# Kernel tuning notes

Hardware: AMD Instinct MI355X
Metric: run time of the kernel (lower is better)

## Reference

```python
import jax, jax.numpy as jnp
import numpy as np

N = 50000        # nodes
E = 400000       # edges
SC = 64          # scalar (l=0) channels
VC = 32          # vector (l=1) channels
DIM = SC + 3 * VC  # 160
NB = 64          # radial basis functions
CUTOFF = 5.0
EPS = 1e-5


def _edge_rot_mat(edge_vec, edge_rand):
    # init_edge_rot_mat: build per-edge frame aligning edge dir with canonical axis
    dist = jnp.sqrt(jnp.sum(edge_vec ** 2, axis=1, keepdims=True))
    nx = edge_vec / dist
    ev2 = edge_rand - 0.5
    ev2 = ev2 / jnp.sqrt(jnp.sum(ev2 ** 2, axis=1, keepdims=True))
    ev2b = jnp.stack([-ev2[:, 1], ev2[:, 0], ev2[:, 2]], axis=1)
    ev2c = jnp.stack([ev2[:, 0], -ev2[:, 2], ev2[:, 1]], axis=1)
    dot = lambda a: jnp.abs(jnp.sum(a * nx, axis=1, keepdims=True))
    ev2 = jnp.where(dot(ev2) > dot(ev2b), ev2b, ev2)
    ev2 = jnp.where(dot(ev2) > dot(ev2c), ev2c, ev2)
    nz = jnp.cross(nx, ev2)
    nz = nz / jnp.sqrt(jnp.sum(nz ** 2, axis=1, keepdims=True))
    ny = jnp.cross(nx, nz)
    ny = ny / jnp.sqrt(jnp.sum(ny ** 2, axis=1, keepdims=True))
    # edge_rot_mat_inv columns = [nz, nx, -ny]; R = inv^T -> rows = [nz, nx, -ny]
    return jnp.stack([nz, nx, -ny], axis=1)  # [E,3,3]


def setup_inputs() -> dict:
    key = jax.random.key(0)
    ks = jax.random.split(key, 10)
    x = jax.random.normal(ks[0], (N, DIM), dtype=jnp.float32)
    pos = jax.random.normal(ks[1], (N, 3), dtype=jnp.float32)
    src = jax.random.randint(ks[2], (E,), 0, N)
    off = jax.random.randint(ks[3], (E,), 1, N)
    dst = (src + off) % N  # no self loops -> nonzero edge vectors
    edge_index = jnp.stack([src, dst], axis=0).astype(jnp.int64)
    edge_rand = jax.random.uniform(ks[4], (E, 3), dtype=jnp.float32)
    W0 = jax.random.normal(ks[5], (SC, SC), dtype=jnp.float32)
    W1 = jax.random.normal(ks[6], (VC, VC), dtype=jnp.float32)
    rbf_centers = jnp.linspace(0.0, CUTOFF, NB).astype(jnp.float32)
    rbf_widths = 0.5 * jnp.ones((NB,), dtype=jnp.float32)
    edge_proj_w = 0.1 * jax.random.normal(ks[7], (NB, 1), dtype=jnp.float32)
    edge_proj_b = jnp.zeros((1,), dtype=jnp.float32)
    ln_gamma = jnp.ones((SC,), dtype=jnp.float32) + 0.1 * jax.random.normal(ks[8], (SC,), dtype=jnp.float32)
    ln_beta = 0.1 * jax.random.normal(ks[9], (SC,), dtype=jnp.float32)
    return {"x": x, "pos": pos, "edge_index": edge_index, "edge_rand": edge_rand,
            "W0": W0, "W1": W1, "rbf_centers": rbf_centers, "rbf_widths": rbf_widths,
            "edge_proj_w": edge_proj_w, "edge_proj_b": edge_proj_b,
            "ln_gamma": ln_gamma, "ln_beta": ln_beta}


def reference(x, pos, edge_index, edge_rand, W0, W1, rbf_centers, rbf_widths,
              edge_proj_w, edge_proj_b, ln_gamma, ln_beta):
    src, dst = edge_index[0], edge_index[1]
    edge_vec = pos[src] - pos[dst]                       # [E,3]
    dist = jnp.sqrt(jnp.sum(edge_vec ** 2, axis=1))      # [E]
    # rotation matrices are detached in the original
    R = jax.lax.stop_gradient(_edge_rot_mat(edge_vec, edge_rand))  # [E,3,3]

    # radial basis (gaussian) with cosine cutoff envelope
    d = dist[:, None]                                    # [E,1]
    rbf = jnp.exp(-0.5 * ((d - rbf_centers) / rbf_widths) ** 2)  # [E,NB]
    cut = jnp.where(d <= CUTOFF, 0.5 * (jnp.cos(jnp.pi * d / CUTOFF) + 1.0), 0.0)
    rbf = rbf * cut                                      # [E,NB]

    # gather source features, split irreps 64x0e + 32x1e
    h = x[src]                                           # [E,DIM]
    h0 = h[:, :SC]                                       # [E,SC]
    h1 = h[:, SC:].reshape(-1, VC, 3)                    # [E,VC,3]

    # rotate l=1 block into the edge-aligned frame (Wigner-D for l=1 is R)
    h1r = jnp.einsum('eij,ecj->eci', R, h1)

    # SO2 convolution: per-l channel mixing (o3.Linear, 1/sqrt(fan_in) path norm)
    m0 = (h0 @ W0) / np.sqrt(SC)                         # [E,SC]
    m1 = jnp.einsum('ecj,cd->edj', h1r, W1) / np.sqrt(VC)  # [E,VC,3]

    # edge modulation: global mean of sigmoid(edge_proj(rbf)) (scalar, as in source)
    edge_w = jnp.mean(jax.nn.sigmoid(rbf @ edge_proj_w + edge_proj_b))
    m0 = m0 * edge_w
    m1 = m1 * edge_w

    # rotate l=1 back with R^T
    m1b = jnp.einsum('eji,ecj->eci', R, m1)
    msg = jnp.concatenate([m0, m1b.reshape(-1, 3 * VC)], axis=1)  # [E,DIM]

    # scatter-sum aggregation over destination nodes
    agg = jax.ops.segment_sum(msg, dst, num_segments=x.shape[0])  # [N,DIM]

    # EquivariantLayerNormV2: LayerNorm on l=0 slice only
    s = agg[:, :SC]
    mu = jnp.mean(s, axis=-1, keepdims=True)
    var = jnp.mean((s - mu) ** 2, axis=-1, keepdims=True)
    s_ln = (s - mu) / jnp.sqrt(var + EPS) * ln_gamma + ln_beta

    # S2Activation: SiLU on l=0 slice, identity on l=1
    s_act = jax.nn.silu(s_ln)
    return jnp.concatenate([s_act, agg[:, SC:]], axis=1)  # [N,DIM]
```

## Files before the change

### kernel.cpp

```cpp
#include <hip/hip_runtime.h>

#define N_NODES 50000
#define N_EDGES 400000
#define DIM 160
#define NB 64
#define CUTOFF 5.0f
#define LN_EPS 1e-5f
#define PI_F 3.14159265358979323846f

#define SLOT_STRIDE 64
#define DEG_STRIDE 4

#define WS_DEG   16
#define WS_PKT   (WS_DEG + N_NODES * DEG_STRIDE)
#define WS_POS4  (WS_PKT + 4 * NB)
#define WS_ESRC  (WS_POS4 + 4 * N_NODES)

__global__ __launch_bounds__(256) void prep(
    const float* __restrict__ pos, const float* __restrict__ centers,
    const float* __restrict__ widths, const float* __restrict__ proj_w,
    int* __restrict__ degp, float4* __restrict__ pkt,
    float4* __restrict__ pos4, float* __restrict__ ew_accum)
{
    const int i = blockIdx.x * blockDim.x + threadIdx.x;
    if (i < 16) ((int*)ew_accum)[i] = 0;
    if (i < NB)
        pkt[i] = make_float4(centers[i], 1.0f / widths[i], proj_w[i], 0.0f);
    if (i < N_NODES) {
        ((int4*)(degp))[i] = make_int4(0, 0, 0, 0);
        pos4[i] = make_float4(pos[3 * i], pos[3 * i + 1], pos[3 * i + 2], 0.0f);
    }
}

#define EPT 4

__global__ __launch_bounds__(256) void hist_ew_fill(
    const int* __restrict__ ei, const float4* __restrict__ pos4,
    const float4* __restrict__ pkt, const float* __restrict__ proj_b,
    int* __restrict__ degp, int* __restrict__ esrc, float* __restrict__ ew_accum)
{
    const float bias = proj_b[0];
    const int base = blockIdx.x * (256 * EPT) + threadIdx.x;

    int  s[EPT], d[EPT], slot[EPT];
    bool v[EPT];
    #pragma unroll
    for (int k = 0; k < EPT; ++k) {
        const int e = base + 256 * k;
        v[k] = (e < N_EDGES);
        s[k] = v[k] ? ei[e] : 0;
        d[k] = v[k] ? ei[N_EDGES + e] : 0;
    }

    #pragma unroll
    for (int k = 0; k < EPT; ++k)
        slot[k] = v[k] ? atomicAdd(&degp[(long)d[k] * DEG_STRIDE], 1) : 0;

    float4 ps[EPT], pd[EPT];
    #pragma unroll
    for (int k = 0; k < EPT; ++k) { ps[k] = pos4[s[k]]; pd[k] = pos4[d[k]]; }

    #pragma unroll
    for (int k = 0; k < EPT; ++k)
        if (v[k] && slot[k] < SLOT_STRIDE)
            esrc[((long)d[k] << 6) + slot[k]] = s[k];

    float dist[EPT];
    #pragma unroll
    for (int k = 0; k < EPT; ++k) {
        const float dx = ps[k].x - pd[k].x;
        const float dy = ps[k].y - pd[k].y;
        const float dz = ps[k].z - pd[k].z;
        dist[k] = sqrtf(dx * dx + dy * dy + dz * dz);
    }

    float z[EPT] = {0.f, 0.f, 0.f, 0.f};
    #pragma unroll 4
    for (int b = 0; b < NB; ++b) {
        const float4 t4 = pkt[b];
        #pragma unroll
        for (int k = 0; k < EPT; ++k) {
            const float t = (dist[k] - t4.x) * t4.y;
            z[k] = fmaf(__expf(-0.5f * t * t), t4.z, z[k]);
        }
    }

    float sig = 0.0f;
    #pragma unroll
    for (int k = 0; k < EPT; ++k) {
        if (v[k]) {
            const float cut = (dist[k] <= CUTOFF)
                            ? 0.5f * (__cosf(PI_F * dist[k] * (1.0f / CUTOFF)) + 1.0f)
                            : 0.0f;
            sig += 1.0f / (1.0f + __expf(-(z[k] * cut + bias)));
        }
    }

    #pragma unroll
    for (int off = 32; off > 0; off >>= 1) sig += __shfl_xor(sig, off);
    __shared__ float red[4];
    if ((threadIdx.x & 63) == 0) red[threadIdx.x >> 6] = sig;
    __syncthreads();
    if (threadIdx.x == 0)
        atomicAdd(ew_accum, red[0] + red[1] + red[2] + red[3]);
}

#define ROWP 164
#define TNODES 64

__global__ __launch_bounds__(256) void gather_node_fused(
    const float* __restrict__ x, const int* __restrict__ degp,
    const int* __restrict__ esrc, float* __restrict__ out,
    const float* __restrict__ W0, const float* __restrict__ W1,
    const float* __restrict__ ln_gamma, const float* __restrict__ ln_beta,
    const float* __restrict__ ew_accum)
{
    __shared__ float sA[TNODES * ROWP];
    __shared__ float sW0[64 * 64];
    __shared__ float sW1[32 * 32];

    const int t    = threadIdx.x;
    const int lane = t & 63;
    const int w    = t >> 6;
    const int node0 = blockIdx.x * TNODES;

    float4 w0r[4];
    #pragma unroll
    for (int i = 0; i < 4; ++i) w0r[i] = ((const float4*)W0)[t + 256 * i];
    const float4 w1r = ((const float4*)W1)[t];

    #pragma unroll 1
    for (int p = 0; p < 16; p += 2) {
        const int nlA = w * 16 + p;
        const int nlB = nlA + 1;
        const int nA  = node0 + nlA;
        const int nB  = node0 + nlB;
        const long nAc = (nA < N_NODES) ? nA : 0;
        const long nBc = (nB < N_NODES) ? nB : 0;

        const int svA  = esrc[(nAc << 6) + lane];
        const int svB  = esrc[(nBc << 6) + lane];
        const int cntA = (nA < N_NODES) ? min(degp[nAc * DEG_STRIDE], SLOT_STRIDE) : 0;
        const int cntB = (nB < N_NODES) ? min(degp[nBc * DEG_STRIDE], SLOT_STRIDE) : 0;

        float4 aA = make_float4(0.f, 0.f, 0.f, 0.f);
        float4 aB = make_float4(0.f, 0.f, 0.f, 0.f);

        #define GBODY(sv, cnt, acc)                                            \
        {                                                                      \
            int j = 0;                                                         \
            for (; j + 8 <= cnt; j += 8) {                                     \
                const int s0 = __shfl(sv, j);                                  \
                const int s1 = __shfl(sv, j + 1);                              \
                const int s2 = __shfl(sv, j + 2);                              \
                const int s3 = __shfl(sv, j + 3);                              \
                const int s4 = __shfl(sv, j + 4);                              \
                const int s5 = __shfl(sv, j + 5);                              \
                const int s6 = __shfl(sv, j + 6);                              \
                const int s7 = __shfl(sv, j + 7);                              \
                if (lane < 40) {                                               \
                    const float4 v0 = ((const float4*)(x + (long)s0 * DIM))[lane]; \
                    const float4 v1 = ((const float4*)(x + (long)s1 * DIM))[lane]; \
                    const float4 v2 = ((const float4*)(x + (long)s2 * DIM))[lane]; \
                    const float4 v3 = ((const float4*)(x + (long)s3 * DIM))[lane]; \
                    const float4 v4 = ((const float4*)(x + (long)s4 * DIM))[lane]; \
                    const float4 v5 = ((const float4*)(x + (long)s5 * DIM))[lane]; \
                    const float4 v6 = ((const float4*)(x + (long)s6 * DIM))[lane]; \
                    const float4 v7 = ((const float4*)(x + (long)s7 * DIM))[lane]; \
                    acc.x += ((v0.x + v1.x) + (v2.x + v3.x)) + ((v4.x + v5.x) + (v6.x + v7.x)); \
                    acc.y += ((v0.y + v1.y) + (v2.y + v3.y)) + ((v4.y + v5.y) + (v6.y + v7.y)); \
                    acc.z += ((v0.z + v1.z) + (v2.z + v3.z)) + ((v4.z + v5.z) + (v6.z + v7.z)); \
                    acc.w += ((v0.w + v1.w) + (v2.w + v3.w)) + ((v4.w + v5.w) + (v6.w + v7.w)); \
                }                                                              \
            }                                                                  \
            for (; j + 4 <= cnt; j += 4) {                                     \
                const int s0 = __shfl(sv, j);                                  \
                const int s1 = __shfl(sv, j + 1);                              \
                const int s2 = __shfl(sv, j + 2);                              \
                const int s3 = __shfl(sv, j + 3);                              \
                if (lane < 40) {                                               \
                    const float4 v0 = ((const float4*)(x + (long)s0 * DIM))[lane]; \
                    const float4 v1 = ((const float4*)(x + (long)s1 * DIM))[lane]; \
                    const float4 v2 = ((const float4*)(x + (long)s2 * DIM))[lane]; \
                    const float4 v3 = ((const float4*)(x + (long)s3 * DIM))[lane]; \
                    acc.x += (v0.x + v1.x) + (v2.x + v3.x);                    \
                    acc.y += (v0.y + v1.y) + (v2.y + v3.y);                    \
                    acc.z += (v0.z + v1.z) + (v2.z + v3.z);                    \
                    acc.w += (v0.w + v1.w) + (v2.w + v3.w);                    \
                }                                                              \
            }                                                                  \
            for (; j < cnt; ++j) {                                             \
                const int s0 = __shfl(sv, j);                                  \
                if (lane < 40) {                                               \
                    const float4 v0 = ((const float4*)(x + (long)s0 * DIM))[lane]; \
                    acc.x += v0.x; acc.y += v0.y; acc.z += v0.z; acc.w += v0.w; \
                }                                                              \
            }                                                                  \
        }
        GBODY(svA, cntA, aA)
        GBODY(svB, cntB, aB)
        #undef GBODY

        if (lane < 40) {
            *(float4*)(&sA[nlA * ROWP + 4 * lane]) = aA;
            *(float4*)(&sA[nlB * ROWP + 4 * lane]) = aB;
        }
    }

    {
        float4* s04 = (float4*)sW0;
        #pragma unroll
        for (int i = 0; i < 4; ++i) s04[t + 256 * i] = w0r[i];
        ((float4*)sW1)[t] = w1r;
    }
    __syncthreads();

    const float ew   = ew_accum[0] * (1.0f / 400000.0f);
    const float s_m0 = ew * 0.125f;
    const float s_m1 = ew * 0.17677669529663687f;

    {
        const int q   = t >> 4;
        const int sub = t & 15;
        const float* r0 = sA + (4 * q + 0) * ROWP;
        const float* r1 = sA + (4 * q + 1) * ROWP;
        const float* r2 = sA + (4 * q + 2) * ROWP;
        const float* r3 = sA + (4 * q + 3) * ROWP;

        float acc[4][4];
        #pragma unroll
        for (int n = 0; n < 4; ++n)
            #pragma unroll
            for (int j = 0; j < 4; ++j) acc[n][j] = 0.0f;

        #pragma unroll 4
        for (int k0 = 0; k0 < 64; k0 += 4) {
            const float4 a0 = *(const float4*)(r0 + k0);
            const float4 a1 = *(const float4*)(r1 + k0);
            const float4 a2 = *(const float4*)(r2 + k0);
            const float4 a3 = *(const float4*)(r3 + k0);
            const float4 w0 = *(const float4*)(sW0 + (k0 + 0) * 64 + 4 * sub);
            const float4 w1 = *(const float4*)(sW0 + (k0 + 1) * 64 + 4 * sub);
            const float4 w2 = *(const float4*)(sW0 + (k0 + 2) * 64 + 4 * sub);
            const float4 w3 = *(const float4*)(sW0 + (k0 + 3) * 64 + 4 * sub);
            #define FMA4(A, av, wv) \
                A[0] = fmaf(av, wv.x, A[0]); A[1] = fmaf(av, wv.y, A[1]); \
                A[2] = fmaf(av, wv.z, A[2]); A[3] = fmaf(av, wv.w, A[3]);
            FMA4(acc[0], a0.x, w0) FMA4(acc[0], a0.y, w1) FMA4(acc[0], a0.z, w2) FMA4(acc[0], a0.w, w3)
            FMA4(acc[1], a1.x, w0) FMA4(acc[1], a1.y, w1) FMA4(acc[1], a1.z, w2) FMA4(acc[1], a1.w, w3)
            FMA4(acc[2], a2.x, w0) FMA4(acc[2], a2.y, w1) FMA4(acc[2], a2.z, w2) FMA4(acc[2], a2.w, w3)
            FMA4(acc[3], a3.x, w0) FMA4(acc[3], a3.y, w1) FMA4(acc[3], a3.z, w2) FMA4(acc[3], a3.w, w3)
            #undef FMA4
        }

        float sum[4], ssq[4];
        #pragma unroll
        for (int n = 0; n < 4; ++n) {
            sum[n] = 0.0f; ssq[n] = 0.0f;
            #pragma unroll
            for (int j = 0; j < 4; ++j) {
                acc[n][j] *= s_m0;
                sum[n] += acc[n][j];
                ssq[n] = fmaf(acc[n][j], acc[n][j], ssq[n]);
            }
        }
        #pragma unroll
        for (int m = 1; m <= 8; m <<= 1) {
            #pragma unroll
            for (int n = 0; n < 4; ++n) {
                sum[n] += __shfl_xor(sum[n], m);
                ssq[n] += __shfl_xor(ssq[n], m);
            }
        }

        const float4 g = *(const float4*)(ln_gamma + 4 * sub);
        const float4 b = *(const float4*)(ln_beta  + 4 * sub);
        #pragma unroll
        for (int n = 0; n < 4; ++n) {
            const int node = node0 + 4 * q + n;
            if (node < N_NODES) {
                const float mu   = sum[n] * (1.0f / 64.0f);
                const float var  = ssq[n] * (1.0f / 64.0f) - mu * mu;
                const float rstd = rsqrtf(var + LN_EPS);
                const float t0 = (acc[n][0] - mu) * rstd * g.x + b.x;
                const float t1 = (acc[n][1] - mu) * rstd * g.y + b.y;
                const float t2 = (acc[n][2] - mu) * rstd * g.z + b.z;
                const float t3 = (acc[n][3] - mu) * rstd * g.w + b.w;
                float4 o;
                o.x = t0 / (1.0f + __expf(-t0));
                o.y = t1 / (1.0f + __expf(-t1));
                o.z = t2 / (1.0f + __expf(-t2));
                o.w = t3 / (1.0f + __expf(-t3));
                *(float4*)(out + (long)node * DIM + 4 * sub) = o;
            }
        }
    }

    {
        const int nl   = t >> 2;
        const int sub  = t & 3;
        const int node = node0 + nl;
        const bool valid = node < N_NODES;
        float* grow = out + (long)(valid ? node : 0) * DIM;
        const float* aRow = sA + nl * ROWP;

        float o[24];
        #pragma unroll
        for (int m = 0; m < 24; ++m) o[m] = 0.0f;

        const float* bRow = aRow + 64;
        #pragma unroll 2
        for (int tt = 0; tt < 8; ++tt) {
            const float4 v0 = *(const float4*)(bRow + 12 * tt);
            const float4 v1 = *(const float4*)(bRow + 12 * tt + 4);
            const float4 v2 = *(const float4*)(bRow + 12 * tt + 8);
            const float a[12] = { v0.x, v0.y, v0.z, v0.w,
                                  v1.x, v1.y, v1.z, v1.w,
                                  v2.x, v2.y, v2.z, v2.w };
            #pragma unroll
            for (int r = 0; r < 4; ++r) {
                const int cp = 4 * tt + r;
                const float a0 = a[3 * r];
                const float a1 = a[3 * r + 1];
                const float a2 = a[3 * r + 2];
                const float4* w4 = (const float4*)(sW1 + cp * 32 + sub * 8);
                const float4 wA = w4[0];
                const float4 wB = w4[1];
                const float wc[8] = { wA.x, wA.y, wA.z, wA.w, wB.x, wB.y, wB.z, wB.w };
                #pragma unroll
                for (int cc = 0; cc < 8; ++cc) {
                    o[3 * cc]     = fmaf(wc[cc], a0, o[3 * cc]);
                    o[3 * cc + 1] = fmaf(wc[cc], a1, o[3 * cc + 1]);
                    o[3 * cc + 2] = fmaf(wc[cc], a2, o[3 * cc + 2]);
                }
            }
        }

        if (valid) {
            float4* ro4 = (float4*)(grow + 64 + 24 * sub);
            #pragma unroll
            for (int q2 = 0; q2 < 6; ++q2) {
                float4 ov;
                ov.x = o[4 * q2]     * s_m1;
                ov.y = o[4 * q2 + 1] * s_m1;
                ov.z = o[4 * q2 + 2] * s_m1;
                ov.w = o[4 * q2 + 3] * s_m1;
                ro4[q2] = ov;
            }
        }
    }
}

extern "C" void kernel_launch(void* const* d_in, const int* in_sizes, int n_in,
                              void* d_out, int out_size, void* d_ws, size_t ws_size,
                              hipStream_t stream) {
    const float* x       = (const float*)d_in[0];
    const float* pos     = (const float*)d_in[1];
    const int*   ei      = (const int*)d_in[2];
    const float* W0      = (const float*)d_in[4];
    const float* W1      = (const float*)d_in[5];
    const float* centers = (const float*)d_in[6];
    const float* widths  = (const float*)d_in[7];
    const float* proj_w  = (const float*)d_in[8];
    const float* proj_b  = (const float*)d_in[9];
    const float* gamma   = (const float*)d_in[10];
    const float* beta    = (const float*)d_in[11];

    float* out  = (float*)d_out;
    int*   wsi  = (int*)d_ws;
    float* ew   = (float*)d_ws;
    int*   degp = wsi + WS_DEG;
    float4* pkt  = (float4*)(wsi + WS_PKT);
    float4* pos4 = (float4*)(wsi + WS_POS4);
    int*   esrc = wsi + WS_ESRC;

    const int pb = (N_NODES + 255) / 256;
    prep<<<pb, 256, 0, stream>>>(pos, centers, widths, proj_w, degp, pkt, pos4, ew);

    const int eb = (N_EDGES + 256 * EPT - 1) / (256 * EPT);
    hist_ew_fill<<<eb, 256, 0, stream>>>(ei, pos4, pkt, proj_b, degp, esrc, ew);

    const int tiles = (N_NODES + TNODES - 1) / TNODES;
    gather_node_fused<<<tiles, 256, 0, stream>>>(x, degp, esrc, out,
                                                 W0, W1, gamma, beta, ew);
}
```

Baseline: 200.9 us.

## Stage gathered node sums in the output buffer instead of LDS

Drops the 64x164 float shared-memory tile and writes the gathered per-node sums straight into the output rows. The scalar matmul/LayerNorm phase and the vector rotation phase then read them back from global memory, separated by a block fence and barrier. This frees about 42KB of LDS per block so more blocks can be resident to hide gather latency. The cost is extra global reads and writes through cache, and a possible read/write overlap on the same output rows. The degree-counter stride also grows from 4 to 8 ints to spread the atomic counters apart.

```diff
diff --git a/kernel.cpp b/kernel.cpp
--- a/kernel.cpp
+++ b/kernel.cpp
@@ -9,7 +9,7 @@
 #define PI_F 3.14159265358979323846f
 
 #define SLOT_STRIDE 64
-#define DEG_STRIDE 4
+#define DEG_STRIDE 8
 
 #define WS_DEG   16
 #define WS_PKT   (WS_DEG + N_NODES * DEG_STRIDE)
@@ -27,7 +27,9 @@
     if (i < NB)
         pkt[i] = make_float4(centers[i], 1.0f / widths[i], proj_w[i], 0.0f);
     if (i < N_NODES) {
-        ((int4*)(degp))[i] = make_int4(0, 0, 0, 0);
+        const int4 z4 = make_int4(0, 0, 0, 0);
+        ((int4*)(degp))[2 * i]     = z4;
+        ((int4*)(degp))[2 * i + 1] = z4;
         pos4[i] = make_float4(pos[3 * i], pos[3 * i + 1], pos[3 * i + 2], 0.0f);
     }
 }
@@ -105,17 +107,15 @@
         atomicAdd(ew_accum, red[0] + red[1] + red[2] + red[3]);
 }
 
-#define ROWP 164
 #define TNODES 64
 
-__global__ __launch_bounds__(256) void gather_node_fused(
+__global__ __launch_bounds__(256) void gather_node(
     const float* __restrict__ x, const int* __restrict__ degp,
     const int* __restrict__ esrc, float* __restrict__ out,
     const float* __restrict__ W0, const float* __restrict__ W1,
     const float* __restrict__ ln_gamma, const float* __restrict__ ln_beta,
     const float* __restrict__ ew_accum)
 {
-    __shared__ float sA[TNODES * ROWP];
     __shared__ float sW0[64 * 64];
     __shared__ float sW1[32 * 32];
 
@@ -124,10 +124,13 @@
     const int w    = t >> 6;
     const int node0 = blockIdx.x * TNODES;
 
-    float4 w0r[4];
-    #pragma unroll
-    for (int i = 0; i < 4; ++i) w0r[i] = ((const float4*)W0)[t + 256 * i];
-    const float4 w1r = ((const float4*)W1)[t];
+    {
+        const float4* w04 = (const float4*)W0;
+        float4* s04 = (float4*)sW0;
+        #pragma unroll
+        for (int i = 0; i < 4; ++i) s04[t + 256 * i] = w04[t + 256 * i];
+        ((float4*)sW1)[t] = ((const float4*)W1)[t];
+    }
 
     #pragma unroll 1
     for (int p = 0; p < 16; p += 2) {
@@ -202,17 +205,12 @@
         #undef GBODY
 
         if (lane < 40) {
-            *(float4*)(&sA[nlA * ROWP + 4 * lane]) = aA;
-            *(float4*)(&sA[nlB * ROWP + 4 * lane]) = aB;
-        }
-    }
-
-    {
-        float4* s04 = (float4*)sW0;
-        #pragma unroll
-        for (int i = 0; i < 4; ++i) s04[t + 256 * i] = w0r[i];
-        ((float4*)sW1)[t] = w1r;
-    }
+            if (nA < N_NODES) *(float4*)(out + (long)nA * DIM + 4 * lane) = aA;
+            if (nB < N_NODES) *(float4*)(out + (long)nB * DIM + 4 * lane) = aB;
+        }
+    }
+
+    __threadfence_block();
     __syncthreads();
 
     const float ew   = ew_accum[0] * (1.0f / 400000.0f);
@@ -222,10 +220,11 @@
     {
         const int q   = t >> 4;
         const int sub = t & 15;
-        const float* r0 = sA + (4 * q + 0) * ROWP;
-        const float* r1 = sA + (4 * q + 1) * ROWP;
-        const float* r2 = sA + (4 * q + 2) * ROWP;
-        const float* r3 = sA + (4 * q + 3) * ROWP;
+        const int n0  = node0 + 4 * q;
+        const float* r0 = out + (long)((n0 + 0 < N_NODES) ? n0 + 0 : 0) * DIM;
+        const float* r1 = out + (long)((n0 + 1 < N_NODES) ? n0 + 1 : 0) * DIM;
+        const float* r2 = out + (long)((n0 + 2 < N_NODES) ? n0 + 2 : 0) * DIM;
+        const float* r3 = out + (long)((n0 + 3 < N_NODES) ? n0 + 3 : 0) * DIM;
 
         float acc[4][4];
         #pragma unroll
@@ -302,13 +301,12 @@
         const int node = node0 + nl;
         const bool valid = node < N_NODES;
         float* grow = out + (long)(valid ? node : 0) * DIM;
-        const float* aRow = sA + nl * ROWP;
+        const float* bRow = grow + 64;
 
         float o[24];
         #pragma unroll
         for (int m = 0; m < 24; ++m) o[m] = 0.0f;
 
-        const float* bRow = aRow + 64;
         #pragma unroll 2
         for (int tt = 0; tt < 8; ++tt) {
             const float4 v0 = *(const float4*)(bRow + 12 * tt);
@@ -381,6 +379,6 @@
     hist_ew_fill<<<eb, 256, 0, stream>>>(ei, pos4, pkt, proj_b, degp, esrc, ew);
 
     const int tiles = (N_NODES + TNODES - 1) / TNODES;
-    gather_node_fused<<<tiles, 256, 0, stream>>>(x, degp, esrc, out,
-                                                 W0, W1, gamma, beta, ew);
+    gather_node<<<tiles, 256, 0, stream>>>(x, degp, esrc, out,
+                                           W0, W1, gamma, beta, ew);
 }
```

Measured after the change: 191.2 us. -4.8%, faster.
